# Optimization experiments

Hardware: AMD Instinct MI355X
Metric: run time of the kernel (lower is better)

Reference implementation:

```python
import jax, jax.numpy as jnp
import numpy as np

NEG = -1e9
TAU = 1.0
N_SAMPLES = 5
SWEEP = (0.1, 0.5, 5)


def layer_norm(x, g, b, eps=1e-5):
    m = x.mean(-1, keepdims=True)
    v = x.var(-1, keepdims=True)
    return (x - m) / jnp.sqrt(v + eps) * g + b


def entmax15(z):
    # exact 1.5-entmax along last axis (Peters & Martins 2019 sort-based algorithm)
    z = z / 2.0
    zs = jnp.sort(z, axis=-1)[..., ::-1]               # descending
    T = z.shape[-1]
    kk = jnp.arange(1, T + 1, dtype=z.dtype)
    mean = jnp.cumsum(zs, -1) / kk
    mean_sq = jnp.cumsum(zs * zs, -1) / kk
    ss = kk * (mean_sq - mean * mean)
    delta = jnp.clip((1.0 - ss) / kk, 0.0)
    tau = mean - jnp.sqrt(delta)
    support = jnp.sum((tau <= zs).astype(jnp.int32), -1, keepdims=True)  # k_star
    tau_star = jnp.take_along_axis(tau, support - 1, axis=-1)
    return jnp.square(jnp.clip(z - tau_star, 0.0))


def stochastic_topk(key, scores, attn, k, tau, n_samples):
    # vectorized over samples AND batch rows with per-row variable k:
    # threshold = k-th largest perturbed score per row (ties measure-zero w/ gumbel)
    u = jax.random.uniform(key, (n_samples,) + scores.shape)
    noise = -jnp.log(-jnp.log(u + 1e-6) + 1e-6)
    pert = jnp.where(attn[None] == 0, NEG, scores[None] + noise * tau)  # [S,B,T]
    srt = jnp.sort(pert, -1)[..., ::-1]
    idx = jnp.broadcast_to((k - 1)[None, :, None], pert.shape[:2] + (1,))
    thr = jnp.take_along_axis(srt, idx, axis=-1)       # [S,B,1]
    h = (pert >= thr).astype(scores.dtype)
    return h.mean(0)                                   # [B,T]


def pool(tok, attn):
    # masked mean pooling (stand-in for sent_encoder.pool)
    return (tok * attn[..., None]).sum(1) / jnp.clip(attn.sum(1, keepdims=True), 1e-6)


def _forward(ids, embeddings, attn, ln_g, ln_b, W1, b1, W2, b2, emb_table):
    emb = embeddings * attn[..., None]
    h = jax.nn.gelu(layer_norm(emb, ln_g, ln_b) @ W1 + b1, approximate=False)
    scores = (h @ W2 + b2)[..., 0]                     # [B,T]
    scores = jnp.where(attn == 0, NEG, scores)

    tok = emb_table[ids]                               # stand-in token embeddings
    full_rep = jax.lax.stop_gradient(pool(tok, attn))  # torch.no_grad path

    T_eff = attn.sum(1)                                # [B]
    # g_soft is identical across the rho sweep in the original; hoisted here
    g_soft = entmax15(scores / TAU) * attn
    g_soft = g_soft / jnp.clip(g_soft.sum(1, keepdims=True), 1e-6)

    key = jax.random.key(42)
    rhos = np.linspace(*SWEEP)
    g_sweep, loss_sweep, rho_eff_sweep = [], [], []
    recon_sum = jnp.zeros((), embeddings.dtype)
    g = None
    for j, rho in enumerate(rhos):
        k = jnp.maximum((float(rho) * T_eff).astype(jnp.int32), 1)
        g_hard = stochastic_topk(jax.random.fold_in(key, j), scores, attn, k, TAU, N_SAMPLES)
        # straight-through: hard forward, soft (entmax) backward
        g = jax.lax.stop_gradient(g_hard) - jax.lax.stop_gradient(g_soft) + g_soft
        rho_eff_sweep.append(g.sum(1) / T_eff)
        eff_attn = attn * g
        pred_rep = pool(tok, eff_attn)
        l_r = jnp.mean(jnp.square(pred_rep - full_rep))  # recon_loss = MSE stand-in
        recon_sum = recon_sum + l_r
        g_sweep.append(g)
        loss_sweep.append(l_r)
    recon_avg = recon_sum / len(rhos)
    return g, jnp.stack(g_sweep), recon_avg, jnp.stack(loss_sweep), jnp.stack(rho_eff_sweep)


def setup_inputs() -> dict:
    key = jax.random.key(0)
    B, T, D, H, V = 8, 2048, 1024, 1365, 32000
    ks = jax.random.split(key, 8)
    return {
        "ids": jax.random.randint(ks[0], (B, T), 0, V),
        "embeddings": jax.random.normal(ks[1], (B, T, D), jnp.float32),
        "attn": jnp.ones((B, T), jnp.float32),
        "ln_g": jnp.ones((D,), jnp.float32),
        "ln_b": jnp.zeros((D,), jnp.float32),
        "W1": jax.random.normal(ks[2], (D, H), jnp.float32) * 0.02,
        "b1": jnp.zeros((H,), jnp.float32),
        "W2": jax.random.normal(ks[3], (H, 1), jnp.float32) * 0.02,
        "b2": jnp.zeros((1,), jnp.float32),
        "emb_table": jax.random.normal(ks[4], (V, D), jnp.float32) * 0.02,
    }


def reference(ids, embeddings, attn, ln_g, ln_b, W1, b1, W2, b2, emb_table):
    return _forward(ids, embeddings, attn, ln_g, ln_b, W1, b1, W2, b2, emb_table)
```

## Files before the change

### kernel.cpp

```cpp
#include <hip/hip_runtime.h>
#include <math.h>
#include <stdint.h>

#define B_ 8
#define T_ 2048
#define D_ 1024
#define H_ 1365
#define HPAD 1536
#define NTOK (B_*T_)
#define NSAMP 5
#define NRHO 5

typedef float  f32x4  __attribute__((ext_vector_type(4)));
typedef __bf16 bf16x8 __attribute__((ext_vector_type(8)));

#define WS_SCORES 0
#define WS_CNT    (WS_SCORES + NTOK*8)
#define WS_PREDW  (WS_CNT + NRHO*B_*T_*4)
#define WS_FULLW  (WS_PREDW + NRHO*B_*D_*8)
#define WS_SUMEFF (WS_FULLW + B_*D_*8)
#define WS_SUMATT (WS_SUMEFF + NRHO*B_*8)
#define WS_SUMG   (WS_SUMATT + B_*8)
#define WS_ZERO_BYTES (WS_SUMG + NRHO*B_*8)
#define WS_STATS  (WS_SUMG + NRHO*B_*8)
#define WS_W1THI  (WS_STATS + NTOK*8)
#define WS_W1TLO  (WS_W1THI + (size_t)HPAD*D_*2)
#define WS_AHI    (WS_W1TLO + (size_t)HPAD*D_*2)
#define WS_ALO    (WS_AHI + (size_t)NTOK*D_*2)
#define WS_FULL_END (WS_ALO + (size_t)NTOK*D_*2)

#define OUT_G      0
#define OUT_GSW    16384
#define OUT_RECON  98304
#define OUT_LOSS   98305
#define OUT_RHOEFF 98310

__device__ inline unsigned short f2bf(float x) {
    uint32_t u = __float_as_uint(x);
    return (unsigned short)((u + 0x7FFFu + ((u >> 16) & 1u)) >> 16);
}

__launch_bounds__(256)
__global__ void k_w1t(const float* __restrict__ W1, unsigned short* __restrict__ hi,
                      unsigned short* __restrict__ lo)
{
    __shared__ float tile[32][33];
    const int tid = threadIdx.x;
    const int bk = blockIdx.x & 31;
    const int bh = blockIdx.x >> 5;
    const int k0 = bk * 32, h0 = bh * 32;
    const int a = tid & 31, b = tid >> 5;
    #pragma unroll
    for (int i = 0; i < 4; ++i) {
        int k = k0 + b + i * 8;
        int h = h0 + a;
        tile[b + i*8][a] = (h < H_) ? W1[(size_t)k * H_ + h] : 0.0f;
    }
    __syncthreads();
    #pragma unroll
    for (int i = 0; i < 4; ++i) {
        int hrow = h0 + b + i * 8;
        int kcol = k0 + a;
        float v = tile[a][b + i*8];
        unsigned short hb = f2bf(v);
        float hf = __uint_as_float((uint32_t)hb << 16);
        unsigned short lb = f2bf(v - hf);
        size_t dst = (size_t)hrow * D_ + kcol;
        hi[dst] = hb; lo[dst] = lb;
    }
}

__launch_bounds__(256)
__global__ void k_asplit(const float* __restrict__ emb, const float* __restrict__ attn,
                         const float* __restrict__ ln_g, const float* __restrict__ ln_b,
                         unsigned short* __restrict__ ahi, unsigned short* __restrict__ alo)
{
    const int tid = threadIdx.x, l = tid & 63, w = tid >> 6;
    const int t0 = blockIdx.x * 64;
    for (int tk = w; tk < 64; tk += 4) {
        const int tg = t0 + tk;
        const float av = attn[tg];
        const float* row = emb + (size_t)tg * D_;
        float rv[16];
        double s1 = 0.0, s2 = 0.0;
        #pragma unroll
        for (int i = 0; i < 16; ++i) {
            rv[i] = row[i*64 + l];
            double x = (double)rv[i] * (double)av;
            s1 += x; s2 += x * x;
        }
        for (int m = 32; m; m >>= 1) { s1 += __shfl_xor(s1, m); s2 += __shfl_xor(s2, m); }
        double mean = s1 / (double)D_;
        double var  = s2 / (double)D_ - mean * mean;
        double inv  = 1.0 / sqrt(var + 1e-5);
        float sc  = (float)((double)av * inv);
        float nsh = -(float)(mean * inv);
        #pragma unroll
        for (int i = 0; i < 16; ++i) {
            int k = i * 64 + l;
            float t  = fmaf(rv[i], sc, nsh);
            float xn = fmaf(t, ln_g[k], ln_b[k]);
            unsigned short hb = f2bf(xn);
            float hf = __uint_as_float((uint32_t)hb << 16);
            size_t dst = (size_t)tg * D_ + k;
            ahi[dst] = hb;
            alo[dst] = f2bf(xn - hf);
        }
    }
}

__launch_bounds__(256)
__global__ void k_stats(const float* __restrict__ emb, const float* __restrict__ attn,
                        float2* __restrict__ stats)
{
    const int tid = threadIdx.x, l = tid & 63, w = tid >> 6;
    const int t0 = blockIdx.x * 64;
    for (int tk = w; tk < 64; tk += 4) {
        const int tg = t0 + tk;
        const float av = attn[tg];
        const float* row = emb + (size_t)tg * D_;
        double s1 = 0.0, s2 = 0.0;
        #pragma unroll
        for (int i = 0; i < D_/64; ++i) {
            double x = (double)row[i*64 + l] * (double)av;
            s1 += x; s2 += x * x;
        }
        for (int m = 32; m; m >>= 1) { s1 += __shfl_xor(s1, m); s2 += __shfl_xor(s2, m); }
        if (l == 0) {
            double mean = s1 / (double)D_;
            double var  = s2 / (double)D_ - mean * mean;
            double inv  = 1.0 / sqrt(var + 1e-5);
            stats[tg] = make_float2((float)((double)av * inv), (float)(mean * inv));
        }
    }
}

#define HIBUF_U 12288
#define LOBUF_U 12288
#define LORING0 49152
#define KSTEPS 32

__device__ __forceinline__ void gll16(const unsigned short* g, unsigned short* l)
{
    __builtin_amdgcn_global_load_lds((const __attribute__((address_space(1))) void*)g,
                                     (__attribute__((address_space(3))) void*)l, 16, 0, 0);
}

__launch_bounds__(512, 2)
__global__ void k_scores8(const unsigned short* __restrict__ ahi,
                          const unsigned short* __restrict__ alo,
                          const unsigned short* __restrict__ w1thi,
                          const unsigned short* __restrict__ w1tlo,
                          const float* __restrict__ b1, const float* __restrict__ W2,
                          double* __restrict__ scores)
{
    __shared__ __align__(16) unsigned short smem[LORING0 + 2*LOBUF_U];

    const int tid = threadIdx.x;
    const int blk = blockIdx.x;
    const int lin = (blk & 7) * 96 + (blk >> 3);
    const int mm = lin / 6, hh = lin - mm * 6;
    const int t0 = mm * 128;
    const int h0 = hh * 256;

    const int l  = tid & 63, w = tid >> 6;
    const int wr = w >> 2, wcn = w & 3;
    const int lm = l & 15, lq = l >> 4;

    const int lrow  = l >> 2;
    const int lslot = (l & 3) ^ ((l >> 3) & 3);
    const unsigned short* sA_hi  = ahi   + (size_t)(t0 + w*16 + lrow) * D_ + lslot*8;
    const unsigned short* sA_lo  = alo   + (size_t)(t0 + w*16 + lrow) * D_ + lslot*8;
    const unsigned short* sB_hi0 = w1thi + (size_t)(h0 + w*32 + lrow) * D_ + lslot*8;
    const unsigned short* sB_hi1 = sB_hi0 + 16*D_;
    const unsigned short* sB_lo0 = w1tlo + (size_t)(h0 + w*32 + lrow) * D_ + lslot*8;
    const unsigned short* sB_lo1 = sB_lo0 + 16*D_;
    const int dA  = w*512;
    const int dB0 = 4096 + w*1024, dB1 = dB0 + 512;

    const int sw8 = (lq ^ ((lm >> 1) & 3)) * 8;
    int offA[4], offB[4];
    #pragma unroll
    for (int r = 0; r < 4; ++r) offA[r] = (wr*64 + r*16 + lm)*32 + sw8;
    #pragma unroll
    for (int c = 0; c < 4; ++c) offB[c] = 4096 + (wcn*64 + c*16 + lm)*32 + sw8;

    f32x4 acc[4][4];
    #pragma unroll
    for (int r = 0; r < 4; ++r)
        #pragma unroll
        for (int c = 0; c < 4; ++c) acc[r][c] = (f32x4){0.f, 0.f, 0.f, 0.f};

    gll16(sA_hi,       &smem[0*HIBUF_U + dA]);
    gll16(sB_hi0,      &smem[0*HIBUF_U + dB0]);
    gll16(sB_hi1,      &smem[0*HIBUF_U + dB1]);
    gll16(sA_lo,       &smem[LORING0 + dA]);
    gll16(sB_lo0,      &smem[LORING0 + dB0]);
    gll16(sB_lo1,      &smem[LORING0 + dB1]);
    gll16(sA_hi  + 32, &smem[1*HIBUF_U + dA]);
    gll16(sB_hi0 + 32, &smem[1*HIBUF_U + dB0]);
    gll16(sB_hi1 + 32, &smem[1*HIBUF_U + dB1]);
    gll16(sA_hi  + 64, &smem[2*HIBUF_U + dA]);
    gll16(sB_hi0 + 64, &smem[2*HIBUF_U + dB0]);
    gll16(sB_hi1 + 64, &smem[2*HIBUF_U + dB1]);
    asm volatile("s_waitcnt vmcnt(3)" ::: "memory");
    asm volatile("s_barrier" ::: "memory");

    bf16x8 ahp[2][4], bhp[2][4];
    #pragma unroll
    for (int r = 0; r < 4; ++r) ahp[0][r] = *(const bf16x8*)&smem[offA[r]];
    #pragma unroll
    for (int c = 0; c < 4; ++c) bhp[0][c] = *(const bf16x8*)&smem[offB[c]];

    #pragma unroll
    for (int t = 0; t < KSTEPS; ++t) {
        const int cur = t & 1, nxt = (t + 1) & 1;
        const int lobase = LORING0 + (t & 1) * LOBUF_U;
        if (t + 1 < KSTEPS) {
            const int lb = LORING0 + ((t + 1) & 1) * LOBUF_U;
            const int ko = (t + 1) * 32;
            gll16(sA_lo  + ko, &smem[lb + dA]);
            gll16(sB_lo0 + ko, &smem[lb + dB0]);
            gll16(sB_lo1 + ko, &smem[lb + dB1]);
        }
        if (t + 3 < KSTEPS) {
            const int hb = ((t + 3) & 3) * HIBUF_U;
            const int ko = (t + 3) * 32;
            gll16(sA_hi  + ko, &smem[hb + dA]);
            gll16(sB_hi0 + ko, &smem[hb + dB0]);
            gll16(sB_hi1 + ko, &smem[hb + dB1]);
        }
        bf16x8 bl[4], al[4];
        #pragma unroll
        for (int c = 0; c < 4; ++c) bl[c] = *(const bf16x8*)&smem[lobase + offB[c]];
        #pragma unroll
        for (int r = 0; r < 4; ++r) al[r] = *(const bf16x8*)&smem[lobase + offA[r]];
        if (t + 1 < KSTEPS) {
            const int hb = ((t + 1) & 3) * HIBUF_U;
            #pragma unroll
            for (int r = 0; r < 4; ++r) ahp[nxt][r] = *(const bf16x8*)&smem[hb + offA[r]];
            #pragma unroll
            for (int c = 0; c < 4; ++c) bhp[nxt][c] = *(const bf16x8*)&smem[hb + offB[c]];
        }
        __builtin_amdgcn_s_setprio(1);
        #pragma unroll
        for (int r = 0; r < 4; ++r)
            #pragma unroll
            for (int c = 0; c < 4; ++c)
                acc[r][c] = __builtin_amdgcn_mfma_f32_16x16x32_bf16(ahp[cur][r], bhp[cur][c], acc[r][c], 0, 0, 0);
        #pragma unroll
        for (int r = 0; r < 4; ++r)
            #pragma unroll
            for (int c = 0; c < 4; ++c)
                acc[r][c] = __builtin_amdgcn_mfma_f32_16x16x32_bf16(ahp[cur][r], bl[c], acc[r][c], 0, 0, 0);
        #pragma unroll
        for (int r = 0; r < 4; ++r)
            #pragma unroll
            for (int c = 0; c < 4; ++c)
                acc[r][c] = __builtin_amdgcn_mfma_f32_16x16x32_bf16(al[r], bhp[cur][c], acc[r][c], 0, 0, 0);
        __builtin_amdgcn_s_setprio(0);
        if (t < KSTEPS - 3)      asm volatile("s_waitcnt vmcnt(3)" ::: "memory");
        else if (t < KSTEPS - 1) asm volatile("s_waitcnt vmcnt(0)" ::: "memory");
        if (t < KSTEPS - 1)      asm volatile("s_barrier" ::: "memory");
    }

    float b1v[4], w2v[4];
    #pragma unroll
    for (int c = 0; c < 4; ++c) {
        int hg = h0 + wcn*64 + c*16 + lm;
        bool ok = (hg < H_);
        b1v[c] = ok ? b1[hg] : 0.0f;
        w2v[c] = ok ? W2[hg] : 0.0f;
    }
    const float is2 = 0.70710678118654752440f;
    #pragma unroll
    for (int r = 0; r < 4; ++r) {
        #pragma unroll
        for (int i = 0; i < 4; ++i) {
            float ps = 0.0f;
            #pragma unroll
            for (int c = 0; c < 4; ++c) {
                float z  = acc[r][c][i] + b1v[c];
                float gl = 0.5f * z * (1.0f + erff(z * is2));
                ps = fmaf(gl, w2v[c], ps);
            }
            double psd = (double)ps;
            psd += __shfl_xor(psd, 1);
            psd += __shfl_xor(psd, 2);
            psd += __shfl_xor(psd, 4);
            psd += __shfl_xor(psd, 8);
            if (lm == 0)
                atomicAdd(&scores[t0 + wr*64 + r*16 + lq*4 + i], psd);
        }
    }
}

__launch_bounds__(256)
__global__ void k_scores_fb(const float* __restrict__ emb, const float* __restrict__ ln_g,
                            const float* __restrict__ ln_b, const float2* __restrict__ stats,
                            const unsigned short* __restrict__ w1thi,
                            const unsigned short* __restrict__ w1tlo,
                            const float* __restrict__ b1, const float* __restrict__ W2,
                            double* __restrict__ scores)
{
    __shared__ __align__(16) unsigned short sAhi[128*40];
    __shared__ __align__(16) unsigned short sAlo[128*40];
    __shared__ __align__(16) unsigned short sBhi[128*40];
    __shared__ __align__(16) unsigned short sBlo[128*40];
    __shared__ float sS1[128], sS2[128];

    const int tid = threadIdx.x;
    const int blk = blockIdx.x;
    const int xcd = blk & 7, slot = blk >> 3;
    const int lin = xcd * 176 + slot;
    const int tt = lin / 11, hh = lin - tt * 11;
    const int t0 = tt * 128;
    const int h0 = hh * 128;

    if (tid < 128) {
        float2 st = stats[t0 + tid];
        sS1[tid] = st.x; sS2[tid] = st.y;
    }
    f32x4 acc[4][4];
    #pragma unroll
    for (int r = 0; r < 4; ++r)
        #pragma unroll
        for (int c = 0; c < 4; ++c) acc[r][c] = (f32x4){0.f, 0.f, 0.f, 0.f};
    const int l = tid & 63, w = tid >> 6;
    const int lm = l & 15, lq = l >> 4;
    const int wr = (w >> 1) * 64;
    const int wc = (w & 1) * 64;
    __syncthreads();

    for (int kc = 0; kc < D_; kc += 32) {
        #pragma unroll
        for (int r2 = 0; r2 < 2; ++r2) {
            int g = tid + r2 * 256;
            int row = g >> 2, oct = g & 3;
            size_t src = (size_t)(h0 + row) * D_ + kc + oct * 8;
            int dst = row * 40 + oct * 8;
            *(bf16x8*)&sBhi[dst] = *(const bf16x8*)&w1thi[src];
            *(bf16x8*)&sBlo[dst] = *(const bf16x8*)&w1tlo[src];
        }
        #pragma unroll
        for (int r2 = 0; r2 < 2; ++r2) {
            int g = tid + r2 * 256;
            int tk = g >> 2, oct = g & 3;
            int tg = t0 + tk, dg = kc + oct * 8;
            const float* ep = emb + (size_t)tg * D_ + dg;
            float s1 = sS1[tk], ns2 = -sS2[tk];
            union { unsigned short s[8]; bf16x8 v; } hi, lo;
            #pragma unroll
            for (int j = 0; j < 8; ++j) {
                float t  = fmaf(ep[j], s1, ns2);
                float xn = fmaf(t, ln_g[dg + j], ln_b[dg + j]);
                unsigned short hb = f2bf(xn);
                float hf = __uint_as_float((uint32_t)hb << 16);
                hi.s[j] = hb;
                lo.s[j] = f2bf(xn - hf);
            }
            int dst = tk * 40 + oct * 8;
            *(bf16x8*)&sAhi[dst] = hi.v;
            *(bf16x8*)&sAlo[dst] = lo.v;
        }
        __syncthreads();
        bf16x8 ah[4], al[4], bh[4], bl[4];
        #pragma unroll
        for (int r = 0; r < 4; ++r) {
            int off = (wr + r * 16 + lm) * 40 + lq * 8;
            ah[r] = *(const bf16x8*)&sAhi[off];
            al[r] = *(const bf16x8*)&sAlo[off];
        }
        #pragma unroll
        for (int c = 0; c < 4; ++c) {
            int off = (wc + c * 16 + lm) * 40 + lq * 8;
            bh[c] = *(const bf16x8*)&sBhi[off];
            bl[c] = *(const bf16x8*)&sBlo[off];
        }
        #pragma unroll
        for (int r = 0; r < 4; ++r)
            #pragma unroll
            for (int c = 0; c < 4; ++c) {
                acc[r][c] = __builtin_amdgcn_mfma_f32_16x16x32_bf16(ah[r], bh[c], acc[r][c], 0, 0, 0);
                acc[r][c] = __builtin_amdgcn_mfma_f32_16x16x32_bf16(ah[r], bl[c], acc[r][c], 0, 0, 0);
                acc[r][c] = __builtin_amdgcn_mfma_f32_16x16x32_bf16(al[r], bh[c], acc[r][c], 0, 0, 0);
            }
        __syncthreads();
    }
    float b1v[4], w2v[4];
    #pragma unroll
    for (int c = 0; c < 4; ++c) {
        int hg = h0 + wc + c * 16 + lm;
        bool ok = (hg < H_);
        b1v[c] = ok ? b1[hg] : 0.0f;
        w2v[c] = ok ? W2[hg] : 0.0f;
    }
    const float is2 = 0.70710678118654752440f;
    #pragma unroll
    for (int r = 0; r < 4; ++r) {
        #pragma unroll
        for (int i = 0; i < 4; ++i) {
            float ps = 0.0f;
            #pragma unroll
            for (int c = 0; c < 4; ++c) {
                float z  = acc[r][c][i] + b1v[c];
                float gl = 0.5f * z * (1.0f + erff(z * is2));
                ps = fmaf(gl, w2v[c], ps);
            }
            double psd = (double)ps;
            psd += __shfl_xor(psd, 1);
            psd += __shfl_xor(psd, 2);
            psd += __shfl_xor(psd, 4);
            psd += __shfl_xor(psd, 8);
            if (lm == 0)
                atomicAdd(&scores[t0 + wr + r * 16 + lq * 4 + i], psd);
        }
    }
}

__device__ inline void tf2x32(uint32_t k0, uint32_t k1, uint32_t x0, uint32_t x1,
                              uint32_t& o0, uint32_t& o1)
{
    const uint32_t ks2 = k0 ^ k1 ^ 0x1BD11BDAu;
    x0 += k0; x1 += k1;
#define ROT_(v,d) (((v) << (d)) | ((v) >> (32 - (d))))
#define RND_(R) { x0 += x1; x1 = ROT_(x1, R); x1 ^= x0; }
    RND_(13) RND_(15) RND_(26) RND_(6)
    x0 += k1;  x1 += ks2 + 1u;
    RND_(17) RND_(29) RND_(16) RND_(24)
    x0 += ks2; x1 += k0 + 2u;
    RND_(13) RND_(15) RND_(26) RND_(6)
    x0 += k0;  x1 += k1 + 3u;
    RND_(17) RND_(29) RND_(16) RND_(24)
    x0 += k1;  x1 += ks2 + 4u;
    RND_(13) RND_(15) RND_(26) RND_(6)
    x0 += ks2; x1 += k0 + 5u;
    o0 = x0; o1 = x1;
#undef RND_
#undef ROT_
}

__launch_bounds__(256)
__global__ void k_topk(const double* __restrict__ scores, const float* __restrict__ attn,
                       const float* __restrict__ b2, int* __restrict__ cnt)
{
    __shared__ unsigned long long keys[2048];
    __shared__ unsigned int hist[256];
    __shared__ unsigned int wsum[4];
    __shared__ unsigned int selDigit, selBase;
    __shared__ double red[4];

    const int tid = threadIdx.x;
    const int blk = blockIdx.x;
    const int j = blk / 40;
    const int s = (blk % 40) >> 3;
    const int b = blk & 7;

    uint32_t kk0, kk1;
    tf2x32(0u, 42u, 0u, (uint32_t)j, kk0, kk1);

    double tsum = 0.0;
    for (int t = tid; t < T_; t += 256) tsum += (double)attn[b * T_ + t];
    for (int m = 32; m; m >>= 1) tsum += __shfl_xor(tsum, m);
    if ((tid & 63) == 0) red[tid >> 6] = tsum;
    __syncthreads();
    const double Teff = red[0] + red[1] + red[2] + red[3];
    const float rhos[5] = {0.1f, 0.2f, 0.3f, 0.4f, 0.5f};
    int kst = (int)(rhos[j] * (float)Teff);
    if (kst < 1) kst = 1;

    const double bb2 = (double)b2[0];
    #pragma unroll
    for (int r = 0; r < 8; ++r) {
        int t = tid + r * 256;
        int f = (s * 8 + b) * T_ + t;
        uint32_t o0, o1;
        tf2x32(kk0, kk1, 0u, (uint32_t)f, o0, o1);
        uint32_t bits = o0 ^ o1;
        float u = __uint_as_float((bits >> 9) | 0x3f800000u) - 1.0f;
        float a1 = (float)((double)u + (double)1e-6f);
        float la = (float)log((double)a1);
        float m1 = (float)((double)1e-6f - (double)la);
        float lb = (float)log((double)m1);
        float noise = -lb;
        float av = attn[b * T_ + t];
        double pv = (av == 0.0f) ? -1e9 : (scores[b * T_ + t] + bb2 + (double)noise);
        unsigned long long uu = (unsigned long long)__double_as_longlong(pv);
        keys[t] = (uu >> 63) ? ~uu : (uu | 0x8000000000000000ull);
    }
    __syncthreads();

    unsigned long long pfx = 0;
    unsigned int plo = (unsigned int)(2048 - kst);
    const int lane = tid & 63, wv = tid >> 6;
    for (int pass = 0; pass < 8; ++pass) {
        const int shift = 56 - 8 * pass;
        const unsigned long long maskhi = (pass == 0) ? 0ull : (~0ull << (64 - 8 * pass));
        hist[tid] = 0;
        __syncthreads();
        #pragma unroll
        for (int r = 0; r < 8; ++r) {
            unsigned long long kk = keys[tid + r * 256];
            if ((kk & maskhi) == pfx)
                atomicAdd(&hist[(unsigned int)((kk >> shift) & 255ull)], 1u);
        }
        __syncthreads();
        unsigned int own = hist[tid];
        int val = (int)own;
        #pragma unroll
        for (int off = 1; off < 64; off <<= 1) {
            int n = __shfl_up(val, off);
            if (lane >= off) val += n;
        }
        if (lane == 63) wsum[wv] = (unsigned int)val;
        __syncthreads();
        unsigned int woff = 0;
        for (int q = 0; q < wv; ++q) woff += wsum[q];
        unsigned int incl = (unsigned int)val + woff;
        unsigned int excl = incl - own;
        if (own > 0 && plo >= excl && plo < incl) { selDigit = (unsigned int)tid; selBase = excl; }
        __syncthreads();
        pfx |= ((unsigned long long)selDigit << shift);
        plo -= selBase;
        __syncthreads();
    }

    #pragma unroll
    for (int r = 0; r < 8; ++r) {
        int t = tid + r * 256;
        if (keys[t] >= pfx) atomicAdd(&cnt[(j * 8 + b) * T_ + t], 1);
    }
}

__launch_bounds__(256)
__global__ void k_gfin(const int* __restrict__ cnt, const float* __restrict__ attn,
                       float* __restrict__ out, double* __restrict__ sumeff,
                       double* __restrict__ sumatt, double* __restrict__ sumg)
{
    __shared__ double redA[4], redB[4], redC[4];
    const int j = blockIdx.x >> 3, b = blockIdx.x & 7;
    const int tid = threadIdx.x;
    double sg = 0.0, se = 0.0, sa = 0.0;
    for (int t = tid; t < T_; t += 256) {
        int c = cnt[(j * 8 + b) * T_ + t];
        float g  = (float)c / 5.0f;
        float av = attn[b * T_ + t];
        out[OUT_GSW + (j * 8 + b) * T_ + t] = g;
        if (j == 4) out[OUT_G + b * T_ + t] = g;
        sg += (double)g;
        se += (double)(av * g);
        sa += (double)av;
    }
    for (int m = 32; m; m >>= 1) { sg += __shfl_xor(sg, m); se += __shfl_xor(se, m); sa += __shfl_xor(sa, m); }
    if ((tid & 63) == 0) { redA[tid>>6] = sg; redB[tid>>6] = se; redC[tid>>6] = sa; }
    __syncthreads();
    if (tid == 0) {
        sg = redA[0]+redA[1]+redA[2]+redA[3];
        se = redB[0]+redB[1]+redB[2]+redB[3];
        sa = redC[0]+redC[1]+redC[2]+redC[3];
        sumg[j*8+b] = sg; sumeff[j*8+b] = se;
        if (j == 0) sumatt[b] = sa;
        out[OUT_RHOEFF + j*8 + b] = (float)sg / (float)sa;
    }
}

__launch_bounds__(256)
__global__ void k_pool(const int* __restrict__ ids, const float* __restrict__ attn,
                       const float* __restrict__ out, const float* __restrict__ emb_table,
                       double* __restrict__ predw, double* __restrict__ fullw)
{
    __shared__ int   sid[128];
    __shared__ float sw[6][128];
    const int blk = blockIdx.x;
    const int b  = blk >> 6;
    const int dc = (blk >> 4) & 3;
    const int tc = blk & 15;
    const int tid = threadIdx.x;
    const int d = dc * 256 + tid;
    if (tid < 128) {
        int t = tc * 128 + tid;
        sid[tid] = ids[b * T_ + t];
        float av = attn[b * T_ + t];
        sw[0][tid] = av;
        #pragma unroll
        for (int j = 0; j < 5; ++j) {
            float g = out[OUT_GSW + (j * 8 + b) * T_ + t];
            sw[1 + j][tid] = av * g;
        }
    }
    __syncthreads();
    double acc[6] = {0,0,0,0,0,0};
    for (int i = 0; i < 128; ++i) {
        float val = emb_table[(size_t)sid[i] * D_ + d];
        #pragma unroll
        for (int c = 0; c < 6; ++c) acc[c] += (double)(val * sw[c][i]);
    }
    atomicAdd(&fullw[b * D_ + d], acc[0]);
    #pragma unroll
    for (int j = 0; j < 5; ++j)
        atomicAdd(&predw[(j * 8 + b) * D_ + d], acc[1 + j]);
}

__launch_bounds__(256)
__global__ void k_loss(const double* __restrict__ predw, const double* __restrict__ fullw,
                       const double* __restrict__ sumeff, const double* __restrict__ sumatt,
                       float* __restrict__ out)
{
    __shared__ double red[4];
    __shared__ float lr[5];
    const int tid = threadIdx.x;
    for (int j = 0; j < 5; ++j) {
        double p = 0.0;
        for (int i = tid; i < B_ * D_; i += 256) {
            int b = i >> 10;
            double dF = sumatt[b];        if (dF < 1e-6) dF = 1e-6;
            double dE = sumeff[j*8 + b];  if (dE < 1e-6) dE = 1e-6;
            double diff = predw[j * B_ * D_ + i] / dE - fullw[i] / dF;
            p += diff * diff;
        }
        for (int m = 32; m; m >>= 1) p += __shfl_xor(p, m);
        if ((tid & 63) == 0) red[tid >> 6] = p;
        __syncthreads();
        if (tid == 0) {
            double t = red[0] + red[1] + red[2] + red[3];
            lr[j] = (float)(t / (double)(B_ * D_));
            out[OUT_LOSS + j] = lr[j];
        }
        __syncthreads();
    }
    if (tid == 0) {
        float srec = 0.0f;
        for (int j = 0; j < 5; ++j) srec += lr[j];
        out[OUT_RECON] = srec / 5.0f;
    }
}

extern "C" void kernel_launch(void* const* d_in, const int* in_sizes, int n_in,
                              void* d_out, int out_size, void* d_ws, size_t ws_size,
                              hipStream_t stream)
{
    const int*   ids  = (const int*)  d_in[0];
    const float* emb  = (const float*)d_in[1];
    const float* attn = (const float*)d_in[2];
    const float* ln_g = (const float*)d_in[3];
    const float* ln_b = (const float*)d_in[4];
    const float* W1   = (const float*)d_in[5];
    const float* b1   = (const float*)d_in[6];
    const float* W2   = (const float*)d_in[7];
    const float* b2   = (const float*)d_in[8];
    const float* et   = (const float*)d_in[9];
    float* out = (float*)d_out;
    char*  ws  = (char*)d_ws;

    double* scores = (double*)(ws + WS_SCORES);
    int*    cnt    = (int*)   (ws + WS_CNT);
    double* predw  = (double*)(ws + WS_PREDW);
    double* fullw  = (double*)(ws + WS_FULLW);
    double* sumeff = (double*)(ws + WS_SUMEFF);
    double* sumatt = (double*)(ws + WS_SUMATT);
    double* sumg   = (double*)(ws + WS_SUMG);
    float2* stats  = (float2*)(ws + WS_STATS);
    unsigned short* w1thi = (unsigned short*)(ws + WS_W1THI);
    unsigned short* w1tlo = (unsigned short*)(ws + WS_W1TLO);
    unsigned short* ahi   = (unsigned short*)(ws + WS_AHI);
    unsigned short* alo   = (unsigned short*)(ws + WS_ALO);

    hipMemsetAsync(d_ws, 0, WS_ZERO_BYTES, stream);

    k_w1t<<<48*32, 256, 0, stream>>>(W1, w1thi, w1tlo);
    if (ws_size >= WS_FULL_END) {
        k_asplit<<<NTOK/64, 256, 0, stream>>>(emb, attn, ln_g, ln_b, ahi, alo);
        k_scores8<<<768, 512, 0, stream>>>(ahi, alo, w1thi, w1tlo, b1, W2, scores);
    } else {
        k_stats<<<NTOK/64, 256, 0, stream>>>(emb, attn, stats);
        k_scores_fb<<<1408, 256, 0, stream>>>(emb, ln_g, ln_b, stats, w1thi, w1tlo,
                                              b1, W2, scores);
    }
    k_topk<<<NRHO * NSAMP * B_, 256, 0, stream>>>(scores, attn, b2, cnt);
    k_gfin<<<NRHO * B_, 256, 0, stream>>>(cnt, attn, out, sumeff, sumatt, sumg);
    k_pool<<<512, 256, 0, stream>>>(ids, attn, out, et, predw, fullw);
    k_loss<<<1, 256, 0, stream>>>(predw, fullw, sumeff, sumatt, out);
}
```

Before: 489.5 us.

## Load W1 operand tiles directly into registers instead of staging through LDS

The split-bf16 scores GEMM no longer stages W1 (hi/lo) tiles through shared memory. Each wave now loads its B fragments straight from global memory into a register double buffer, and only the A (activation hi/lo) tiles stay in a 4-deep LDS ring. This shrinks the LDS footprint and cuts LDS traffic and global_load_lds instructions. In exchange, each wave issues redundant uncoalesced global loads of W1 (the four waves sharing a column group reload the same data) and holds more registers, which risks exposed latency inside the loop. The vmcnt waits also change, since they now have to account for the direct register loads.

```diff
diff --git a/kernel.cpp b/kernel.cpp
--- a/kernel.cpp
+++ b/kernel.cpp
@@ -135,9 +135,7 @@
     }
 }
 
-#define HIBUF_U 12288
-#define LOBUF_U 12288
-#define LORING0 49152
+#define ABUF_U 8192
 #define KSTEPS 32
 
 __device__ __forceinline__ void gll16(const unsigned short* g, unsigned short* l)
@@ -154,7 +152,7 @@
                           const float* __restrict__ b1, const float* __restrict__ W2,
                           double* __restrict__ scores)
 {
-    __shared__ __align__(16) unsigned short smem[LORING0 + 2*LOBUF_U];
+    __shared__ __align__(16) unsigned short smem[4*ABUF_U];
 
     const int tid = threadIdx.x;
     const int blk = blockIdx.x;
@@ -169,21 +167,17 @@
 
     const int lrow  = l >> 2;
     const int lslot = (l & 3) ^ ((l >> 3) & 3);
-    const unsigned short* sA_hi  = ahi   + (size_t)(t0 + w*16 + lrow) * D_ + lslot*8;
-    const unsigned short* sA_lo  = alo   + (size_t)(t0 + w*16 + lrow) * D_ + lslot*8;
-    const unsigned short* sB_hi0 = w1thi + (size_t)(h0 + w*32 + lrow) * D_ + lslot*8;
-    const unsigned short* sB_hi1 = sB_hi0 + 16*D_;
-    const unsigned short* sB_lo0 = w1tlo + (size_t)(h0 + w*32 + lrow) * D_ + lslot*8;
-    const unsigned short* sB_lo1 = sB_lo0 + 16*D_;
-    const int dA  = w*512;
-    const int dB0 = 4096 + w*1024, dB1 = dB0 + 512;
+    const unsigned short* sA_hi = ahi + (size_t)(t0 + w*16 + lrow) * D_ + lslot*8;
+    const unsigned short* sA_lo = alo + (size_t)(t0 + w*16 + lrow) * D_ + lslot*8;
+    const int dA = w*512;
 
     const int sw8 = (lq ^ ((lm >> 1) & 3)) * 8;
-    int offA[4], offB[4];
+    int offA[4];
     #pragma unroll
     for (int r = 0; r < 4; ++r) offA[r] = (wr*64 + r*16 + lm)*32 + sw8;
-    #pragma unroll
-    for (int c = 0; c < 4; ++c) offB[c] = 4096 + (wcn*64 + c*16 + lm)*32 + sw8;
+
+    const unsigned short* bBh = w1thi + (size_t)(h0 + wcn*64 + lm) * D_ + lq*8;
+    const unsigned short* bBl = w1tlo + (size_t)(h0 + wcn*64 + lm) * D_ + lq*8;
 
     f32x4 acc[4][4];
     #pragma unroll
@@ -191,56 +185,48 @@
         #pragma unroll
         for (int c = 0; c < 4; ++c) acc[r][c] = (f32x4){0.f, 0.f, 0.f, 0.f};
 
-    gll16(sA_hi,       &smem[0*HIBUF_U + dA]);
-    gll16(sB_hi0,      &smem[0*HIBUF_U + dB0]);
-    gll16(sB_hi1,      &smem[0*HIBUF_U + dB1]);
-    gll16(sA_lo,       &smem[LORING0 + dA]);
-    gll16(sB_lo0,      &smem[LORING0 + dB0]);
-    gll16(sB_lo1,      &smem[LORING0 + dB1]);
-    gll16(sA_hi  + 32, &smem[1*HIBUF_U + dA]);
-    gll16(sB_hi0 + 32, &smem[1*HIBUF_U + dB0]);
-    gll16(sB_hi1 + 32, &smem[1*HIBUF_U + dB1]);
-    gll16(sA_hi  + 64, &smem[2*HIBUF_U + dA]);
-    gll16(sB_hi0 + 64, &smem[2*HIBUF_U + dB0]);
-    gll16(sB_hi1 + 64, &smem[2*HIBUF_U + dB1]);
-    asm volatile("s_waitcnt vmcnt(3)" ::: "memory");
+    gll16(sA_hi,      &smem[0*ABUF_U + dA]);
+    gll16(sA_lo,      &smem[0*ABUF_U + dA + 4096]);
+    gll16(sA_hi + 32, &smem[1*ABUF_U + dA]);
+    gll16(sA_lo + 32, &smem[1*ABUF_U + dA + 4096]);
+    gll16(sA_hi + 64, &smem[2*ABUF_U + dA]);
+    gll16(sA_lo + 64, &smem[2*ABUF_U + dA + 4096]);
+    bf16x8 ahp[2][4], alp[2][4], bhp[2][4], blp[2][4];
+    #pragma unroll
+    for (int c = 0; c < 4; ++c) {
+        bhp[0][c] = *(const bf16x8*)&bBh[(size_t)c*16*D_];
+        blp[0][c] = *(const bf16x8*)&bBl[(size_t)c*16*D_];
+    }
+    asm volatile("s_waitcnt vmcnt(0)" ::: "memory");
     asm volatile("s_barrier" ::: "memory");
-
-    bf16x8 ahp[2][4], bhp[2][4];
-    #pragma unroll
-    for (int r = 0; r < 4; ++r) ahp[0][r] = *(const bf16x8*)&smem[offA[r]];
-    #pragma unroll
-    for (int c = 0; c < 4; ++c) bhp[0][c] = *(const bf16x8*)&smem[offB[c]];
+    #pragma unroll
+    for (int r = 0; r < 4; ++r) {
+        ahp[0][r] = *(const bf16x8*)&smem[offA[r]];
+        alp[0][r] = *(const bf16x8*)&smem[4096 + offA[r]];
+    }
 
     #pragma unroll
     for (int t = 0; t < KSTEPS; ++t) {
         const int cur = t & 1, nxt = (t + 1) & 1;
-        const int lobase = LORING0 + (t & 1) * LOBUF_U;
         if (t + 1 < KSTEPS) {
-            const int lb = LORING0 + ((t + 1) & 1) * LOBUF_U;
-            const int ko = (t + 1) * 32;
-            gll16(sA_lo  + ko, &smem[lb + dA]);
-            gll16(sB_lo0 + ko, &smem[lb + dB0]);
-            gll16(sB_lo1 + ko, &smem[lb + dB1]);
+            #pragma unroll
+            for (int c = 0; c < 4; ++c) {
+                bhp[nxt][c] = *(const bf16x8*)&bBh[(size_t)c*16*D_ + (t+1)*32];
+                blp[nxt][c] = *(const bf16x8*)&bBl[(size_t)c*16*D_ + (t+1)*32];
+            }
         }
         if (t + 3 < KSTEPS) {
-            const int hb = ((t + 3) & 3) * HIBUF_U;
-            const int ko = (t + 3) * 32;
-            gll16(sA_hi  + ko, &smem[hb + dA]);
-            gll16(sB_hi0 + ko, &smem[hb + dB0]);
-            gll16(sB_hi1 + ko, &smem[hb + dB1]);
-        }
-        bf16x8 bl[4], al[4];
-        #pragma unroll
-        for (int c = 0; c < 4; ++c) bl[c] = *(const bf16x8*)&smem[lobase + offB[c]];
-        #pragma unroll
-        for (int r = 0; r < 4; ++r) al[r] = *(const bf16x8*)&smem[lobase + offA[r]];
+            const int ab = ((t + 3) & 3) * ABUF_U;
+            gll16(sA_hi + (t+3)*32, &smem[ab + dA]);
+            gll16(sA_lo + (t+3)*32, &smem[ab + dA + 4096]);
+        }
         if (t + 1 < KSTEPS) {
-            const int hb = ((t + 1) & 3) * HIBUF_U;
-            #pragma unroll
-            for (int r = 0; r < 4; ++r) ahp[nxt][r] = *(const bf16x8*)&smem[hb + offA[r]];
-            #pragma unroll
-            for (int c = 0; c < 4; ++c) bhp[nxt][c] = *(const bf16x8*)&smem[hb + offB[c]];
+            const int ab = ((t + 1) & 3) * ABUF_U;
+            #pragma unroll
+            for (int r = 0; r < 4; ++r) {
+                ahp[nxt][r] = *(const bf16x8*)&smem[ab + offA[r]];
+                alp[nxt][r] = *(const bf16x8*)&smem[ab + 4096 + offA[r]];
+            }
         }
         __builtin_amdgcn_s_setprio(1);
         #pragma unroll
@@ -252,16 +238,16 @@
         for (int r = 0; r < 4; ++r)
             #pragma unroll
             for (int c = 0; c < 4; ++c)
-                acc[r][c] = __builtin_amdgcn_mfma_f32_16x16x32_bf16(ahp[cur][r], bl[c], acc[r][c], 0, 0, 0);
+                acc[r][c] = __builtin_amdgcn_mfma_f32_16x16x32_bf16(ahp[cur][r], blp[cur][c], acc[r][c], 0, 0, 0);
         #pragma unroll
         for (int r = 0; r < 4; ++r)
             #pragma unroll
             for (int c = 0; c < 4; ++c)
-                acc[r][c] = __builtin_amdgcn_mfma_f32_16x16x32_bf16(al[r], bhp[cur][c], acc[r][c], 0, 0, 0);
+                acc[r][c] = __builtin_amdgcn_mfma_f32_16x16x32_bf16(alp[cur][r], bhp[cur][c], acc[r][c], 0, 0, 0);
         __builtin_amdgcn_s_setprio(0);
-        if (t < KSTEPS - 3)      asm volatile("s_waitcnt vmcnt(3)" ::: "memory");
-        else if (t < KSTEPS - 1) asm volatile("s_waitcnt vmcnt(0)" ::: "memory");
-        if (t < KSTEPS - 1)      asm volatile("s_barrier" ::: "memory");
+        if (t < KSTEPS - 3) asm volatile("s_waitcnt vmcnt(2)" ::: "memory");
+        else                asm volatile("s_waitcnt vmcnt(0)" ::: "memory");
+        if (t < KSTEPS - 1) asm volatile("s_barrier" ::: "memory");
     }
 
     float b1v[4], w2v[4];
```

New measurement: 594.9 us. 21.5% more time.
